# Kernel optimization log

Hardware: AMD Instinct MI355X
Metric: run time of the kernel (lower is better)

## Reference

```python
import jax, jax.numpy as jnp
import numpy as np

B, N_PER, D_IN, D_OUT, E_PER = 64, 256, 256, 128, 8192  # graphs, nodes/graph, in feat, out feat (=clusters K), edges/graph
EPS = 1e-12


def _sage(h, src, dst, W, b):
    # DenseSAGEConv (mean aggregator): h [n,Din], src/dst [E]
    agg = jnp.zeros_like(h).at[dst].add(h[src])                 # sum of in-neighbor messages
    deg = jnp.zeros((h.shape[0],), h.dtype).at[dst].add(1.0)
    agg = agg / jnp.maximum(deg, 1.0)[:, None]                  # mean aggregation
    z = jnp.concatenate([h, agg], axis=-1) @ W + b              # Linear(2*Din -> Dout)
    z = z / jnp.maximum(jnp.linalg.norm(z, axis=-1, keepdims=True), EPS)  # F.normalize(p=2)
    return jax.nn.relu(z)                                       # activation


def setup_inputs() -> dict:
    key = jax.random.key(0)
    ks = jax.random.split(key, 5)
    h = jax.random.normal(ks[0], (B, N_PER, D_IN), jnp.float32)
    edge_src = jax.random.randint(ks[1], (B, E_PER), 0, N_PER)
    edge_dst = jax.random.randint(ks[2], (B, E_PER), 0, N_PER)
    s = 1.0 / np.sqrt(2 * D_IN)
    W_feat = jax.random.uniform(ks[3], (2 * D_IN, D_OUT), jnp.float32, -s, s)
    b_feat = jnp.zeros((D_OUT,), jnp.float32)
    W_pool = jax.random.uniform(ks[4], (2 * D_IN, D_OUT), jnp.float32, -s, s)
    b_pool = jnp.zeros((D_OUT,), jnp.float32)
    return {"h": h, "edge_src": edge_src, "edge_dst": edge_dst,
            "W_feat": W_feat, "b_feat": b_feat, "W_pool": W_pool, "b_pool": b_pool}


def reference(h, edge_src, edge_dst, W_feat, b_feat, W_pool, b_pool):
    sage = jax.vmap(_sage, in_axes=(0, 0, 0, None, None))
    feat = sage(h, edge_src, edge_dst, W_feat, b_feat)                          # [B,n,K]
    assign = jax.nn.softmax(sage(h, edge_src, edge_dst, W_pool, b_pool), -1)    # [B,n,K]
    # h = assign^T @ feat, per graph (equivalent to block_diag(assign)^T @ stacked feat)
    h_pool = jnp.einsum('bnk,bnd->bkd', assign, feat).reshape(B * D_OUT, D_OUT)  # [B*K, Dout]
    # adj_new = S^T A S per graph; A[dst,src]=1 per edge -> sum_e outer(S[dst_e], S[src_e])
    s_dst = jnp.take_along_axis(assign, edge_dst[:, :, None], axis=1)           # [B,E,K]
    s_src = jnp.take_along_axis(assign, edge_src[:, :, None], axis=1)           # [B,E,K]
    blocks = jnp.einsum('bek,bel->bkl', s_dst, s_src)                           # [B,K,K]
    # cross-graph blocks are exactly zero in the batched graph -> block-diagonal dense adj
    adj_new = jax.scipy.linalg.block_diag(*blocks)                              # [B*K, B*K]
    return adj_new, h_pool
```

## Files before the change

kernel.cpp:

```cpp
#include <hip/hip_runtime.h>
#include <hip/hip_bf16.h>
#include <stdint.h>

#define BG 64
#define NP 256
#define DI 256
#define DO 128
#define EP 8192


__device__ __forceinline__ int ldi(const void* p, size_t i, int i64) {
  return i64 ? (int)((const long long*)p)[i] : ((const int*)p)[i];
}

__global__ __launch_bounds__(256) void k_scatter(const void* __restrict__ esrc,
                                                 const void* __restrict__ edst,
                                                 float* __restrict__ A,
                                                 float* __restrict__ deg) {
  __shared__ int cnt;
  int b = blockIdx.x, t = threadIdx.x;
  if (t == 0) cnt = 0;
  __syncthreads();
  uint32_t w = ((const uint32_t*)esrc)[2 * t + 1];
  if (w != 0) atomicAdd(&cnt, 1);
  float4* Az = (float4*)(A + (size_t)b * NP * NP);
  for (int i = t; i < NP * NP / 4; i += 256) Az[i] = make_float4(0.f, 0.f, 0.f, 0.f);
  deg[b * NP + t] = 0.f;
  __syncthreads();
  int i64 = (cnt == 0);
  const size_t base = (size_t)b * EP;
  float* Ab = A + (size_t)b * NP * NP;
  float* degb = deg + b * NP;
  for (int e = t; e < EP; e += 256) {
    int si = ldi(esrc, base + e, i64) & (NP - 1);
    int di = ldi(edst, base + e, i64) & (NP - 1);
    atomicAdd(Ab + (size_t)di * NP + si, 1.0f);
    atomicAdd(degb + di, 1.0f);
  }
}

__global__ __launch_bounds__(256) void k_gemm_agg(const float* __restrict__ A,
                                                  const float* __restrict__ h,
                                                  const float* __restrict__ deg,
                                                  float* __restrict__ agg) {
  __shared__ __align__(16) float As[32][68];
  __shared__ __align__(16) float Hs[32][132];
  int b = blockIdx.y;
  int r0 = (blockIdx.x & 3) * 64;
  int f0 = (blockIdx.x >> 2) * 128;
  int t = threadIdx.x;
  int tr = t >> 4, tc = t & 15;
  float acc[4][8] = {};
  const float* Ab = A + (size_t)b * NP * NP;
  const float* hb = h + (size_t)b * NP * DI;
  for (int kc = 0; kc < NP; kc += 32) {
    __syncthreads();
    {
      int r = t >> 2;
      int ks = (t & 3) * 8;
      const float* src = &Ab[(size_t)(r0 + r) * NP + kc + ks];
      float4 v0 = *(const float4*)src;
      float4 v1 = *(const float4*)(src + 4);
      As[ks + 0][r] = v0.x; As[ks + 1][r] = v0.y; As[ks + 2][r] = v0.z; As[ks + 3][r] = v0.w;
      As[ks + 4][r] = v1.x; As[ks + 5][r] = v1.y; As[ks + 6][r] = v1.z; As[ks + 7][r] = v1.w;
    }
    {
      int k = t >> 3;
      int fs = (t & 7) * 16;
      const float* src = &hb[(size_t)(kc + k) * DI + f0 + fs];
#pragma unroll
      for (int j = 0; j < 4; ++j)
        *(float4*)&Hs[k][fs + j * 4] = *(const float4*)(src + j * 4);
    }
    __syncthreads();
#pragma unroll
    for (int k = 0; k < 32; ++k) {
      float a[4], ww[8];
      *(float4*)&a[0] = *(const float4*)&As[k][tr * 4];
      *(float4*)&ww[0] = *(const float4*)&Hs[k][tc * 8];
      *(float4*)&ww[4] = *(const float4*)&Hs[k][tc * 8 + 4];
#pragma unroll
      for (int i = 0; i < 4; ++i)
#pragma unroll
        for (int j = 0; j < 8; ++j)
          acc[i][j] += a[i] * ww[j];
    }
  }
#pragma unroll
  for (int i = 0; i < 4; ++i) {
    int gi = r0 + tr * 4 + i;
    float sc = 1.0f / fmaxf(deg[b * NP + gi], 1.0f);
    float* dst = &agg[((size_t)b * NP + gi) * DI + f0 + tc * 8];
    float o0[4] = { acc[i][0] * sc, acc[i][1] * sc, acc[i][2] * sc, acc[i][3] * sc };
    float o1[4] = { acc[i][4] * sc, acc[i][5] * sc, acc[i][6] * sc, acc[i][7] * sc };
    *(float4*)dst = *(float4*)o0;
    *(float4*)(dst + 4) = *(float4*)o1;
  }
}

__global__ __launch_bounds__(256) void k_gemm_zepi(const float* __restrict__ h,
                                                   const float* __restrict__ agg,
                                                   const float* __restrict__ Wf,
                                                   const float* __restrict__ Wp,
                                                   const float* __restrict__ bfe,
                                                   const float* __restrict__ bpo,
                                                   float* __restrict__ feat,
                                                   float* __restrict__ assign) {
  __shared__ __align__(16) float Xs[32][36];
  __shared__ __align__(16) float Ws[32][264];
  int r0 = blockIdx.x * 32;
  int t = threadIdx.x;
  int rg = t >> 5;
  int cg = t & 31;
  float acc[4][8] = {};
  for (int kc = 0; kc < 2 * DI; kc += 32) {
    __syncthreads();
    {
      int r = t >> 3;
      int kk = (t & 7) * 4;
      const float* src = (kc < DI) ? &h[(size_t)(r0 + r) * DI + kc + kk]
                                   : &agg[(size_t)(r0 + r) * DI + (kc - DI) + kk];
      float4 v = *(const float4*)src;
      Xs[kk + 0][r] = v.x; Xs[kk + 1][r] = v.y; Xs[kk + 2][r] = v.z; Xs[kk + 3][r] = v.w;
    }
    {
      int k = t >> 3;
      int cbase = (t & 7) * 32;
      const float* srcW = (cbase < DO) ? &Wf[(size_t)(kc + k) * DO + cbase]
                                       : &Wp[(size_t)(kc + k) * DO + cbase - DO];
#pragma unroll
      for (int j = 0; j < 8; ++j)
        *(float4*)&Ws[k][cbase + j * 4] = *(const float4*)(srcW + j * 4);
    }
    __syncthreads();
#pragma unroll
    for (int kk = 0; kk < 32; ++kk) {
      float a[4], ww[8];
      *(float4*)&a[0] = *(const float4*)&Xs[kk][rg * 4];
      *(float4*)&ww[0] = *(const float4*)&Ws[kk][cg * 8];
      *(float4*)&ww[4] = *(const float4*)&Ws[kk][cg * 8 + 4];
#pragma unroll
      for (int i = 0; i < 4; ++i)
#pragma unroll
        for (int j = 0; j < 8; ++j)
          acc[i][j] += a[i] * ww[j];
    }
  }
  int half = cg >> 4;
  float bias[8];
  {
    const float* bp = half ? bpo : bfe;
#pragma unroll
    for (int j = 0; j < 8; ++j) bias[j] = bp ? bp[(cg * 8 + j) & (DO - 1)] : 0.f;
  }
#pragma unroll
  for (int i = 0; i < 4; ++i) {
    int r = r0 + rg * 4 + i;
    float z[8];
    float ss = 0.f;
#pragma unroll
    for (int j = 0; j < 8; ++j) { z[j] = acc[i][j] + bias[j]; ss += z[j] * z[j]; }
    ss += __shfl_xor(ss, 1); ss += __shfl_xor(ss, 2);
    ss += __shfl_xor(ss, 4); ss += __shfl_xor(ss, 8);
    float inv = 1.0f / fmaxf(sqrtf(ss), 1e-12f);
    float v[8];
#pragma unroll
    for (int j = 0; j < 8; ++j) v[j] = fmaxf(z[j] * inv, 0.f);
    if (half == 0) {
      float* dst = &feat[(size_t)r * DO + cg * 8];
      *(float4*)dst = *(float4*)&v[0];
      *(float4*)(dst + 4) = *(float4*)&v[4];
    } else {
      float mx = v[0];
#pragma unroll
      for (int j = 1; j < 8; ++j) mx = fmaxf(mx, v[j]);
      mx = fmaxf(mx, __shfl_xor(mx, 1)); mx = fmaxf(mx, __shfl_xor(mx, 2));
      mx = fmaxf(mx, __shfl_xor(mx, 4)); mx = fmaxf(mx, __shfl_xor(mx, 8));
      float e[8], s = 0.f;
#pragma unroll
      for (int j = 0; j < 8; ++j) { e[j] = __expf(v[j] - mx); s += e[j]; }
      s += __shfl_xor(s, 1); s += __shfl_xor(s, 2);
      s += __shfl_xor(s, 4); s += __shfl_xor(s, 8);
      float is = 1.0f / s;
      float o[8];
#pragma unroll
      for (int j = 0; j < 8; ++j) o[j] = e[j] * is;
      float* dst = &assign[(size_t)r * DO + (cg - 16) * 8];
      *(float4*)dst = *(float4*)&o[0];
      *(float4*)(dst + 4) = *(float4*)&o[4];
    }
  }
}

__global__ __launch_bounds__(256) void k_gemm_as(const float* __restrict__ A,
                                                 const float* __restrict__ assign,
                                                 float* __restrict__ AS) {
  __shared__ __align__(16) float As[32][68];
  __shared__ __align__(16) float Bs[32][132];
  int b = blockIdx.y;
  int r0 = blockIdx.x * 64;
  int t = threadIdx.x;
  int tr = t >> 4, tc = t & 15;
  float acc[4][8] = {};
  const float* Ab = A + (size_t)b * NP * NP;
  const float* asb = assign + (size_t)b * NP * DO;
  for (int kc = 0; kc < NP; kc += 32) {
    __syncthreads();
    {
      int r = t >> 2;
      int ks = (t & 3) * 8;
      const float* src = &Ab[(size_t)(r0 + r) * NP + kc + ks];
      float4 v0 = *(const float4*)src;
      float4 v1 = *(const float4*)(src + 4);
      As[ks + 0][r] = v0.x; As[ks + 1][r] = v0.y; As[ks + 2][r] = v0.z; As[ks + 3][r] = v0.w;
      As[ks + 4][r] = v1.x; As[ks + 5][r] = v1.y; As[ks + 6][r] = v1.z; As[ks + 7][r] = v1.w;
    }
    {
      int k = t >> 3;
      int ls = (t & 7) * 16;
      const float* src = &asb[(size_t)(kc + k) * DO + ls];
#pragma unroll
      for (int j = 0; j < 4; ++j)
        *(float4*)&Bs[k][ls + j * 4] = *(const float4*)(src + j * 4);
    }
    __syncthreads();
#pragma unroll
    for (int k = 0; k < 32; ++k) {
      float a[4], ww[8];
      *(float4*)&a[0] = *(const float4*)&As[k][tr * 4];
      *(float4*)&ww[0] = *(const float4*)&Bs[k][tc * 8];
      *(float4*)&ww[4] = *(const float4*)&Bs[k][tc * 8 + 4];
#pragma unroll
      for (int i = 0; i < 4; ++i)
#pragma unroll
        for (int j = 0; j < 8; ++j)
          acc[i][j] += a[i] * ww[j];
    }
  }
#pragma unroll
  for (int i = 0; i < 4; ++i) {
    float* dst = &AS[((size_t)b * NP + r0 + tr * 4 + i) * DO + tc * 8];
    *(float4*)dst = *(float4*)&acc[i][0];
    *(float4*)(dst + 4) = *(float4*)&acc[i][4];
  }
}

__global__ __launch_bounds__(256) void k_pool(const float* __restrict__ assign,
                                              const float* __restrict__ AS,
                                              const float* __restrict__ feat,
                                              float* __restrict__ adj,
                                              float* __restrict__ hpool) {
  __shared__ __align__(16) float Ps[32][68];
  __shared__ __align__(16) float Ys[32][132];
  int b = blockIdx.y;
  int mt = blockIdx.x & 1;
  int which = blockIdx.x >> 1;
  const float* Y = which ? feat : AS;
  int m0 = mt * 64;
  int t = threadIdx.x;
  int tr = t >> 4, tc = t & 15;
  float acc[4][8] = {};
  for (int nc = 0; nc < NP; nc += 32) {
    __syncthreads();
    {
      int n = t >> 3;
      int mseg = (t & 7) * 8;
      const float* src = &assign[((size_t)b * NP + nc + n) * DO + m0 + mseg];
      *(float4*)&Ps[n][mseg] = *(const float4*)src;
      *(float4*)&Ps[n][mseg + 4] = *(const float4*)(src + 4);
    }
    {
      int n = t >> 3;
      int ds = (t & 7) * 16;
      const float* src = &Y[((size_t)b * NP + nc + n) * DO + ds];
#pragma unroll
      for (int j = 0; j < 4; ++j)
        *(float4*)&Ys[n][ds + j * 4] = *(const float4*)(src + j * 4);
    }
    __syncthreads();
#pragma unroll
    for (int n = 0; n < 32; ++n) {
      float a[4], ww[8];
      *(float4*)&a[0] = *(const float4*)&Ps[n][tr * 4];
      *(float4*)&ww[0] = *(const float4*)&Ys[n][tc * 8];
      *(float4*)&ww[4] = *(const float4*)&Ys[n][tc * 8 + 4];
#pragma unroll
      for (int i = 0; i < 4; ++i)
#pragma unroll
        for (int j = 0; j < 8; ++j)
          acc[i][j] += a[i] * ww[j];
    }
  }
  if (which == 0) {
#pragma unroll
    for (int i = 0; i < 4; ++i) {
      float* dst = &adj[(size_t)(b * DO + m0 + tr * 4 + i) * (BG * DO) + b * DO + tc * 8];
      *(float4*)dst = *(float4*)&acc[i][0];
      *(float4*)(dst + 4) = *(float4*)&acc[i][4];
    }
  } else {
#pragma unroll
    for (int i = 0; i < 4; ++i) {
      float* dst = &hpool[((size_t)b * DO + m0 + tr * 4 + i) * DO + tc * 8];
      *(float4*)dst = *(float4*)&acc[i][0];
      *(float4*)(dst + 4) = *(float4*)&acc[i][4];
    }
  }
}

extern "C" void kernel_launch(void* const* d_in, const int* in_sizes, int n_in,
                              void* d_out, int out_size, void* d_ws, size_t ws_size,
                              hipStream_t stream) {
  (void)out_size; (void)ws_size;
  int ih = -1, ie[2] = {-1, -1}, iw[2] = {-1, -1}, ib[2] = {-1, -1};
  int ne = 0, nw = 0, nb = 0;
  for (int i = 0; i < n_in; ++i) {
    long long s = in_sizes[i];
    if (s == (long long)BG * NP * DI) { if (ih < 0) ih = i; }
    else if (s == (long long)BG * EP && ne < 2) ie[ne++] = i;
    else if (s == (long long)2 * DI * DO && nw < 2) iw[nw++] = i;
    else if (s == (long long)DO && nb < 2) ib[nb++] = i;
  }
  if (ih < 0 || ne < 2 || nw < 2) {
    ih = 0;
    ie[0] = (n_in > 1) ? 1 : 0;  ie[1] = (n_in > 2) ? 2 : ie[0];
    iw[0] = (n_in > 3) ? 3 : 0;  iw[1] = (n_in > 5) ? 5 : iw[0];
    ib[0] = (n_in > 4) ? 4 : -1; ib[1] = (n_in > 6) ? 6 : -1;
    nb = (ib[1] >= 0) ? 2 : (ib[0] >= 0 ? 1 : 0);
  }
  const float* h    = (const float*)d_in[ih];
  const void* esrc  = d_in[ie[0]];
  const void* edst  = d_in[ie[1]];
  const float* Wf   = (const float*)d_in[iw[0]];
  const float* Wp   = (const float*)d_in[iw[1]];
  const float* bfe  = (nb >= 1) ? (const float*)d_in[ib[0]] : nullptr;
  const float* bpo  = (nb >= 2) ? (const float*)d_in[ib[1]] : nullptr;

  float* adj   = (float*)d_out;
  float* hpool = (float*)d_out + (size_t)(BG * DO) * (BG * DO);
  const size_t ADJ_BYTES = (size_t)(BG * DO) * (BG * DO) * sizeof(float);

  char* wb = (char*)d_ws;
  float* A      = (float*)wb;
  float* agg    = (float*)(wb + 16777216);
  float* feat   = (float*)(wb + 33554432);
  float* assign = (float*)(wb + 41943040);
  float* AS     = (float*)(wb + 50331648);
  float* deg    = (float*)(wb + 58720256);

  hipMemsetAsync(adj, 0, ADJ_BYTES, stream);
  k_scatter<<<BG, 256, 0, stream>>>(esrc, edst, A, deg);
  k_gemm_agg<<<dim3(8, BG), 256, 0, stream>>>(A, h, deg, agg);
  k_gemm_zepi<<<BG * NP / 32, 256, 0, stream>>>(h, agg, Wf, Wp, bfe, bpo, feat, assign);
  k_gemm_as<<<dim3(4, BG), 256, 0, stream>>>(A, assign, AS);
  k_pool<<<dim3(4, BG), 256, 0, stream>>>(assign, AS, feat, adj, hpool);
}
```

Baseline: 508.0 us.

## Halve GEMM tiles for more blocks, fuse adj zeroing into pool, LDS degree atomics

Every GEMM kernel now uses 32-row tiles with 2x8 per-thread microtiles instead of 64x 4x8, doubling grid sizes. zepi also splits its two heads across separate blocks. The separate memset of the 256MB block-diagonal adj output is removed; pool blocks now write their full output rows, zeros included, from LDS-staged results. Degree counting moves to shared-memory atomics. Smaller tiles raise occupancy and block count but lower arithmetic intensity per LDS load.

```diff
diff --git a/kernel.cpp b/kernel.cpp
--- a/kernel.cpp
+++ b/kernel.cpp
@@ -18,51 +18,50 @@
                                                  float* __restrict__ A,
                                                  float* __restrict__ deg) {
   __shared__ int cnt;
+  __shared__ float sdeg[NP];
   int b = blockIdx.x, t = threadIdx.x;
   if (t == 0) cnt = 0;
+  sdeg[t] = 0.f;
   __syncthreads();
   uint32_t w = ((const uint32_t*)esrc)[2 * t + 1];
   if (w != 0) atomicAdd(&cnt, 1);
   float4* Az = (float4*)(A + (size_t)b * NP * NP);
   for (int i = t; i < NP * NP / 4; i += 256) Az[i] = make_float4(0.f, 0.f, 0.f, 0.f);
-  deg[b * NP + t] = 0.f;
   __syncthreads();
   int i64 = (cnt == 0);
   const size_t base = (size_t)b * EP;
   float* Ab = A + (size_t)b * NP * NP;
-  float* degb = deg + b * NP;
   for (int e = t; e < EP; e += 256) {
     int si = ldi(esrc, base + e, i64) & (NP - 1);
     int di = ldi(edst, base + e, i64) & (NP - 1);
     atomicAdd(Ab + (size_t)di * NP + si, 1.0f);
-    atomicAdd(degb + di, 1.0f);
-  }
+    atomicAdd(&sdeg[di], 1.0f);
+  }
+  __syncthreads();
+  deg[b * NP + t] = sdeg[t];
 }
 
 __global__ __launch_bounds__(256) void k_gemm_agg(const float* __restrict__ A,
                                                   const float* __restrict__ h,
                                                   const float* __restrict__ deg,
                                                   float* __restrict__ agg) {
-  __shared__ __align__(16) float As[32][68];
+  __shared__ __align__(16) float As[32][36];
   __shared__ __align__(16) float Hs[32][132];
   int b = blockIdx.y;
-  int r0 = (blockIdx.x & 3) * 64;
-  int f0 = (blockIdx.x >> 2) * 128;
+  int r0 = (blockIdx.x & 7) * 32;
+  int f0 = (blockIdx.x >> 3) * 128;
   int t = threadIdx.x;
   int tr = t >> 4, tc = t & 15;
-  float acc[4][8] = {};
+  float acc[2][8] = {};
   const float* Ab = A + (size_t)b * NP * NP;
   const float* hb = h + (size_t)b * NP * DI;
   for (int kc = 0; kc < NP; kc += 32) {
     __syncthreads();
     {
-      int r = t >> 2;
-      int ks = (t & 3) * 8;
-      const float* src = &Ab[(size_t)(r0 + r) * NP + kc + ks];
-      float4 v0 = *(const float4*)src;
-      float4 v1 = *(const float4*)(src + 4);
-      As[ks + 0][r] = v0.x; As[ks + 1][r] = v0.y; As[ks + 2][r] = v0.z; As[ks + 3][r] = v0.w;
-      As[ks + 4][r] = v1.x; As[ks + 5][r] = v1.y; As[ks + 6][r] = v1.z; As[ks + 7][r] = v1.w;
+      int r = t >> 3;
+      int ks = (t & 7) * 4;
+      float4 v = *(const float4*)&Ab[(size_t)(r0 + r) * NP + kc + ks];
+      As[ks + 0][r] = v.x; As[ks + 1][r] = v.y; As[ks + 2][r] = v.z; As[ks + 3][r] = v.w;
     }
     {
       int k = t >> 3;
@@ -75,26 +74,24 @@
     __syncthreads();
 #pragma unroll
     for (int k = 0; k < 32; ++k) {
-      float a[4], ww[8];
-      *(float4*)&a[0] = *(const float4*)&As[k][tr * 4];
+      float a0 = As[k][tr * 2], a1 = As[k][tr * 2 + 1];
+      float ww[8];
       *(float4*)&ww[0] = *(const float4*)&Hs[k][tc * 8];
       *(float4*)&ww[4] = *(const float4*)&Hs[k][tc * 8 + 4];
 #pragma unroll
-      for (int i = 0; i < 4; ++i)
-#pragma unroll
-        for (int j = 0; j < 8; ++j)
-          acc[i][j] += a[i] * ww[j];
-    }
-  }
-#pragma unroll
-  for (int i = 0; i < 4; ++i) {
-    int gi = r0 + tr * 4 + i;
+      for (int j = 0; j < 8; ++j) { acc[0][j] += a0 * ww[j]; acc[1][j] += a1 * ww[j]; }
+    }
+  }
+#pragma unroll
+  for (int i = 0; i < 2; ++i) {
+    int gi = r0 + tr * 2 + i;
     float sc = 1.0f / fmaxf(deg[b * NP + gi], 1.0f);
+    float o[8];
+#pragma unroll
+    for (int j = 0; j < 8; ++j) o[j] = acc[i][j] * sc;
     float* dst = &agg[((size_t)b * NP + gi) * DI + f0 + tc * 8];
-    float o0[4] = { acc[i][0] * sc, acc[i][1] * sc, acc[i][2] * sc, acc[i][3] * sc };
-    float o1[4] = { acc[i][4] * sc, acc[i][5] * sc, acc[i][6] * sc, acc[i][7] * sc };
-    *(float4*)dst = *(float4*)o0;
-    *(float4*)(dst + 4) = *(float4*)o1;
+    *(float4*)dst = *(float4*)&o[0];
+    *(float4*)(dst + 4) = *(float4*)&o[4];
   }
 }
 
@@ -107,12 +104,15 @@
                                                    float* __restrict__ feat,
                                                    float* __restrict__ assign) {
   __shared__ __align__(16) float Xs[32][36];
-  __shared__ __align__(16) float Ws[32][264];
-  int r0 = blockIdx.x * 32;
+  __shared__ __align__(16) float Ws[32][132];
+  int head = blockIdx.x & 1;
+  int r0 = (blockIdx.x >> 1) * 32;
+  const float* W = head ? Wp : Wf;
+  const float* bp = head ? bpo : bfe;
   int t = threadIdx.x;
-  int rg = t >> 5;
-  int cg = t & 31;
-  float acc[4][8] = {};
+  int rg = t >> 4;
+  int cg = t & 15;
+  float acc[2][8] = {};
   for (int kc = 0; kc < 2 * DI; kc += 32) {
     __syncthreads();
     {
@@ -125,37 +125,29 @@
     }
     {
       int k = t >> 3;
-      int cbase = (t & 7) * 32;
-      const float* srcW = (cbase < DO) ? &Wf[(size_t)(kc + k) * DO + cbase]
-                                       : &Wp[(size_t)(kc + k) * DO + cbase - DO];
-#pragma unroll
-      for (int j = 0; j < 8; ++j)
-        *(float4*)&Ws[k][cbase + j * 4] = *(const float4*)(srcW + j * 4);
-    }
-    __syncthreads();
-#pragma unroll
-    for (int kk = 0; kk < 32; ++kk) {
-      float a[4], ww[8];
-      *(float4*)&a[0] = *(const float4*)&Xs[kk][rg * 4];
-      *(float4*)&ww[0] = *(const float4*)&Ws[kk][cg * 8];
-      *(float4*)&ww[4] = *(const float4*)&Ws[kk][cg * 8 + 4];
-#pragma unroll
-      for (int i = 0; i < 4; ++i)
-#pragma unroll
-        for (int j = 0; j < 8; ++j)
-          acc[i][j] += a[i] * ww[j];
-    }
-  }
-  int half = cg >> 4;
+      int cs = (t & 7) * 16;
+      const float* src = &W[(size_t)(kc + k) * DO + cs];
+#pragma unroll
+      for (int j = 0; j < 4; ++j)
+        *(float4*)&Ws[k][cs + j * 4] = *(const float4*)(src + j * 4);
+    }
+    __syncthreads();
+#pragma unroll
+    for (int k = 0; k < 32; ++k) {
+      float a0 = Xs[k][rg * 2], a1 = Xs[k][rg * 2 + 1];
+      float ww[8];
+      *(float4*)&ww[0] = *(const float4*)&Ws[k][cg * 8];
+      *(float4*)&ww[4] = *(const float4*)&Ws[k][cg * 8 + 4];
+#pragma unroll
+      for (int j = 0; j < 8; ++j) { acc[0][j] += a0 * ww[j]; acc[1][j] += a1 * ww[j]; }
+    }
+  }
   float bias[8];
-  {
-    const float* bp = half ? bpo : bfe;
-#pragma unroll
-    for (int j = 0; j < 8; ++j) bias[j] = bp ? bp[(cg * 8 + j) & (DO - 1)] : 0.f;
-  }
-#pragma unroll
-  for (int i = 0; i < 4; ++i) {
-    int r = r0 + rg * 4 + i;
+#pragma unroll
+  for (int j = 0; j < 8; ++j) bias[j] = bp ? bp[cg * 8 + j] : 0.f;
+#pragma unroll
+  for (int i = 0; i < 2; ++i) {
+    int r = r0 + rg * 2 + i;
     float z[8];
     float ss = 0.f;
 #pragma unroll
@@ -166,7 +158,7 @@
     float v[8];
 #pragma unroll
     for (int j = 0; j < 8; ++j) v[j] = fmaxf(z[j] * inv, 0.f);
-    if (half == 0) {
+    if (head == 0) {
       float* dst = &feat[(size_t)r * DO + cg * 8];
       *(float4*)dst = *(float4*)&v[0];
       *(float4*)(dst + 4) = *(float4*)&v[4];
@@ -185,7 +177,7 @@
       float o[8];
 #pragma unroll
       for (int j = 0; j < 8; ++j) o[j] = e[j] * is;
-      float* dst = &assign[(size_t)r * DO + (cg - 16) * 8];
+      float* dst = &assign[(size_t)r * DO + cg * 8];
       *(float4*)dst = *(float4*)&o[0];
       *(float4*)(dst + 4) = *(float4*)&o[4];
     }
@@ -195,25 +187,22 @@
 __global__ __launch_bounds__(256) void k_gemm_as(const float* __restrict__ A,
                                                  const float* __restrict__ assign,
                                                  float* __restrict__ AS) {
-  __shared__ __align__(16) float As[32][68];
+  __shared__ __align__(16) float As[32][36];
   __shared__ __align__(16) float Bs[32][132];
   int b = blockIdx.y;
-  int r0 = blockIdx.x * 64;
+  int r0 = blockIdx.x * 32;
   int t = threadIdx.x;
   int tr = t >> 4, tc = t & 15;
-  float acc[4][8] = {};
+  float acc[2][8] = {};
   const float* Ab = A + (size_t)b * NP * NP;
   const float* asb = assign + (size_t)b * NP * DO;
   for (int kc = 0; kc < NP; kc += 32) {
     __syncthreads();
     {
-      int r = t >> 2;
-      int ks = (t & 3) * 8;
-      const float* src = &Ab[(size_t)(r0 + r) * NP + kc + ks];
-      float4 v0 = *(const float4*)src;
-      float4 v1 = *(const float4*)(src + 4);
-      As[ks + 0][r] = v0.x; As[ks + 1][r] = v0.y; As[ks + 2][r] = v0.z; As[ks + 3][r] = v0.w;
-      As[ks + 4][r] = v1.x; As[ks + 5][r] = v1.y; As[ks + 6][r] = v1.z; As[ks + 7][r] = v1.w;
+      int r = t >> 3;
+      int ks = (t & 7) * 4;
+      float4 v = *(const float4*)&Ab[(size_t)(r0 + r) * NP + kc + ks];
+      As[ks + 0][r] = v.x; As[ks + 1][r] = v.y; As[ks + 2][r] = v.z; As[ks + 3][r] = v.w;
     }
     {
       int k = t >> 3;
@@ -226,20 +215,17 @@
     __syncthreads();
 #pragma unroll
     for (int k = 0; k < 32; ++k) {
-      float a[4], ww[8];
-      *(float4*)&a[0] = *(const float4*)&As[k][tr * 4];
+      float a0 = As[k][tr * 2], a1 = As[k][tr * 2 + 1];
+      float ww[8];
       *(float4*)&ww[0] = *(const float4*)&Bs[k][tc * 8];
       *(float4*)&ww[4] = *(const float4*)&Bs[k][tc * 8 + 4];
 #pragma unroll
-      for (int i = 0; i < 4; ++i)
-#pragma unroll
-        for (int j = 0; j < 8; ++j)
-          acc[i][j] += a[i] * ww[j];
-    }
-  }
-#pragma unroll
-  for (int i = 0; i < 4; ++i) {
-    float* dst = &AS[((size_t)b * NP + r0 + tr * 4 + i) * DO + tc * 8];
+      for (int j = 0; j < 8; ++j) { acc[0][j] += a0 * ww[j]; acc[1][j] += a1 * ww[j]; }
+    }
+  }
+#pragma unroll
+  for (int i = 0; i < 2; ++i) {
+    float* dst = &AS[((size_t)b * NP + r0 + tr * 2 + i) * DO + tc * 8];
     *(float4*)dst = *(float4*)&acc[i][0];
     *(float4*)(dst + 4) = *(float4*)&acc[i][4];
   }
@@ -250,24 +236,22 @@
                                               const float* __restrict__ feat,
                                               float* __restrict__ adj,
                                               float* __restrict__ hpool) {
-  __shared__ __align__(16) float Ps[32][68];
+  __shared__ __align__(16) float Ps[32][36];
   __shared__ __align__(16) float Ys[32][132];
   int b = blockIdx.y;
-  int mt = blockIdx.x & 1;
-  int which = blockIdx.x >> 1;
+  int which = blockIdx.x & 1;
+  int mt = blockIdx.x >> 1;
   const float* Y = which ? feat : AS;
-  int m0 = mt * 64;
+  int m0 = mt * 32;
   int t = threadIdx.x;
   int tr = t >> 4, tc = t & 15;
-  float acc[4][8] = {};
+  float acc[2][8] = {};
   for (int nc = 0; nc < NP; nc += 32) {
     __syncthreads();
     {
       int n = t >> 3;
-      int mseg = (t & 7) * 8;
-      const float* src = &assign[((size_t)b * NP + nc + n) * DO + m0 + mseg];
-      *(float4*)&Ps[n][mseg] = *(const float4*)src;
-      *(float4*)&Ps[n][mseg + 4] = *(const float4*)(src + 4);
+      int ms = (t & 7) * 4;
+      *(float4*)&Ps[n][ms] = *(const float4*)&assign[((size_t)b * NP + nc + n) * DO + m0 + ms];
     }
     {
       int n = t >> 3;
@@ -280,30 +264,38 @@
     __syncthreads();
 #pragma unroll
     for (int n = 0; n < 32; ++n) {
-      float a[4], ww[8];
-      *(float4*)&a[0] = *(const float4*)&Ps[n][tr * 4];
+      float a0 = Ps[n][tr * 2], a1 = Ps[n][tr * 2 + 1];
+      float ww[8];
       *(float4*)&ww[0] = *(const float4*)&Ys[n][tc * 8];
       *(float4*)&ww[4] = *(const float4*)&Ys[n][tc * 8 + 4];
 #pragma unroll
-      for (int i = 0; i < 4; ++i)
-#pragma unroll
-        for (int j = 0; j < 8; ++j)
-          acc[i][j] += a[i] * ww[j];
-    }
-  }
-  if (which == 0) {
-#pragma unroll
-    for (int i = 0; i < 4; ++i) {
-      float* dst = &adj[(size_t)(b * DO + m0 + tr * 4 + i) * (BG * DO) + b * DO + tc * 8];
+      for (int j = 0; j < 8; ++j) { acc[0][j] += a0 * ww[j]; acc[1][j] += a1 * ww[j]; }
+    }
+  }
+  if (which == 1) {
+#pragma unroll
+    for (int i = 0; i < 2; ++i) {
+      float* dst = &hpool[((size_t)b * DO + m0 + tr * 2 + i) * DO + tc * 8];
       *(float4*)dst = *(float4*)&acc[i][0];
       *(float4*)(dst + 4) = *(float4*)&acc[i][4];
     }
   } else {
-#pragma unroll
-    for (int i = 0; i < 4; ++i) {
-      float* dst = &hpool[((size_t)b * DO + m0 + tr * 4 + i) * DO + tc * 8];
-      *(float4*)dst = *(float4*)&acc[i][0];
-      *(float4*)(dst + 4) = *(float4*)&acc[i][4];
+    __syncthreads();
+#pragma unroll
+    for (int i = 0; i < 2; ++i) {
+      *(float4*)&Ys[tr * 2 + i][tc * 8] = *(float4*)&acc[i][0];
+      *(float4*)&Ys[tr * 2 + i][tc * 8 + 4] = *(float4*)&acc[i][4];
+    }
+    __syncthreads();
+    const int ROWW = BG * DO;
+    for (int row = 0; row < 32; ++row) {
+      float4* base = (float4*)&adj[(size_t)(b * DO + m0 + row) * ROWW];
+      for (int j = t; j < ROWW / 4; j += 256) {
+        float4 v = make_float4(0.f, 0.f, 0.f, 0.f);
+        unsigned off = (unsigned)(j * 4 - b * DO);
+        if (off < (unsigned)DO) v = *(float4*)&Ys[row][off];
+        base[j] = v;
+      }
     }
   }
 }
@@ -338,7 +330,6 @@
 
   float* adj   = (float*)d_out;
   float* hpool = (float*)d_out + (size_t)(BG * DO) * (BG * DO);
-  const size_t ADJ_BYTES = (size_t)(BG * DO) * (BG * DO) * sizeof(float);
 
   char* wb = (char*)d_ws;
   float* A      = (float*)wb;
@@ -348,10 +339,9 @@
   float* AS     = (float*)(wb + 50331648);
   float* deg    = (float*)(wb + 58720256);
 
-  hipMemsetAsync(adj, 0, ADJ_BYTES, stream);
   k_scatter<<<BG, 256, 0, stream>>>(esrc, edst, A, deg);
-  k_gemm_agg<<<dim3(8, BG), 256, 0, stream>>>(A, h, deg, agg);
-  k_gemm_zepi<<<BG * NP / 32, 256, 0, stream>>>(h, agg, Wf, Wp, bfe, bpo, feat, assign);
-  k_gemm_as<<<dim3(4, BG), 256, 0, stream>>>(A, assign, AS);
-  k_pool<<<dim3(4, BG), 256, 0, stream>>>(assign, AS, feat, adj, hpool);
-}
+  k_gemm_agg<<<dim3(16, BG), 256, 0, stream>>>(A, h, deg, agg);
+  k_gemm_zepi<<<2 * BG * NP / 32, 256, 0, stream>>>(h, agg, Wf, Wp, bfe, bpo, feat, assign);
+  k_gemm_as<<<dim3(8, BG), 256, 0, stream>>>(A, assign, AS);
+  k_pool<<<dim3(8, BG), 256, 0, stream>>>(assign, AS, feat, adj, hpool);
+}
```

New measurement: 548.7 us. +8.0%, slower.
